# Kernel tuning notes

Hardware: AMD Instinct MI355X
Metric: run time of the kernel (lower is better)

Reference implementation:

```python
import jax, jax.numpy as jnp
from jax import lax
import numpy as np

WINDOW = 51
HALF = WINDOW // 2  # 25
K_SAUVOLA = 0.2     # skimage threshold_sauvola default k
RGB_W = np.array([0.2989, 0.5870, 0.1140], dtype=np.float32)  # tf.image.rgb_to_grayscale weights


def _window_sum(x, axis):
    """Sliding-window sum of length WINDOW along `axis`, 'same' size, reflect padding.
    O(1) per pixel via cumulative sums (integral-image style), matching the
    uniform_filter-based local statistics in skimage's Sauvola."""
    pad = [(0, 0)] * x.ndim
    pad[axis] = (HALF, HALF)
    xp = jnp.pad(x, pad, mode='reflect')
    cs = jnp.cumsum(xp, axis=axis)
    zshape = list(cs.shape)
    zshape[axis] = 1
    cs = jnp.concatenate([jnp.zeros(zshape, cs.dtype), cs], axis=axis)
    n = cs.shape[axis]
    hi = lax.slice_in_dim(cs, WINDOW, n, axis=axis)
    lo = lax.slice_in_dim(cs, 0, n - WINDOW, axis=axis)
    return hi - lo


def _box_mean(x):
    # separable 51x51 box filter over H (axis 1) and W (axis 2)
    s = _window_sum(_window_sum(x, axis=1), axis=2)
    return s / jnp.asarray(WINDOW * WINDOW, x.dtype)


def setup_inputs() -> dict:
    key = jax.random.key(0)
    inputs = jax.random.uniform(key, (8, 1024, 1024, 3), dtype=jnp.float32)
    return {"inputs": inputs}


def reference(inputs) -> jnp.ndarray:
    # RGB -> grayscale (channels == 3 branch), keep channel dim [B,H,W,1]
    gray = jnp.einsum('bhwc,c->bhw', inputs, jnp.asarray(RGB_W))[..., None]
    # local mean / std over 51x51 window
    m = _box_mean(gray)
    m2 = _box_mean(gray * gray)
    var = jnp.maximum(m2 - m * m, 0.0)
    s = jnp.sqrt(var)
    # skimage default dynamic range: r = 0.5 * (max - min) over the whole array
    r = 0.5 * (jnp.max(gray) - jnp.min(gray))
    thresh = m * (1.0 + K_SAUVOLA * (s / r - 1.0))
    # (gray > thresh) * 1
    return (gray > thresh).astype(jnp.float32)
```

## Files before the change

### kernel.cpp

```cpp
#include <hip/hip_runtime.h>

#define IMW 1024
#define IMH 1024
#define NB  8
#define HALF 25
#define STRIP 16
#define NCELL 64

#define W_R ((double)0.2989f)
#define W_G ((double)0.5870f)
#define W_B ((double)0.1140f)
#define INV_AREA (1.0 / 2601.0)

__device__ __forceinline__ int refl(int i, int n) {
    if (i < 0) i = -i;
    if (i >= n) i = 2 * n - 2 - i;
    return i;
}

__device__ __forceinline__ double wsum(const double* __restrict__ C, int p) {
    int a = p + HALF; if (a > IMW - 1) a = IMW - 1;
    int b = p - HALF - 1;
    double s = C[a] - (b >= 0 ? C[b] : 0.0);
    if (p <= HALF - 1)      s += C[HALF - p] - C[0];
    if (p >= IMW - HALF)    s += C[IMW - 2] - C[2*IMW - 2 - HALF - 1 - p];
    return s;
}

__global__ void k0_init(unsigned* cells) {
    cells[threadIdx.x] = (threadIdx.x < NCELL) ? 0xFFFFFFFFu : 0u;
}

__global__ __launch_bounds__(256) void k1_rowpass(const float* __restrict__ in,
                                                  float2* __restrict__ hp,
                                                  float* __restrict__ gray,
                                                  unsigned* __restrict__ cells) {
    __shared__ double cs1[IMW];
    __shared__ double cs2[IMW];
    __shared__ double wt1[4], wt2[4];
    __shared__ float bmin[4], bmax[4];
    const int row = blockIdx.x;
    const long long base = (long long)row * IMW;
    const int t = threadIdx.x;
    const int lane = t & 63, w = t >> 6;

    const float4* p4 = (const float4*)(in + base * 3);
    float4 f0 = p4[3*t], f1 = p4[3*t+1], f2 = p4[3*t+2];
    double g0 = (double)f0.x*W_R + (double)f0.y*W_G + (double)f0.z*W_B;
    double g1 = (double)f0.w*W_R + (double)f1.x*W_G + (double)f1.y*W_B;
    double g2 = (double)f1.z*W_R + (double)f1.w*W_G + (double)f2.x*W_B;
    double g3 = (double)f2.y*W_R + (double)f2.z*W_G + (double)f2.w*W_B;
    float gf0 = (float)g0, gf1 = (float)g1, gf2 = (float)g2, gf3 = (float)g3;

    ((float4*)(gray + base))[t] = make_float4(gf0, gf1, gf2, gf3);

    double l1_0 = g0, l1_1 = l1_0 + g1, l1_2 = l1_1 + g2, l1_3 = l1_2 + g3;
    double l2_0 = g0*g0, l2_1 = l2_0 + g1*g1, l2_2 = l2_1 + g2*g2, l2_3 = l2_2 + g3*g3;

    float lmin = fminf(fminf(gf0, gf1), fminf(gf2, gf3));
    float lmax = fmaxf(fmaxf(gf0, gf1), fmaxf(gf2, gf3));
    for (int off = 32; off; off >>= 1) {
        lmin = fminf(lmin, __shfl_down(lmin, off));
        lmax = fmaxf(lmax, __shfl_down(lmax, off));
    }
    if (lane == 0) { bmin[w] = lmin; bmax[w] = lmax; }

    double v1 = l1_3, v2 = l2_3;
    for (int off = 1; off < 64; off <<= 1) {
        double u1 = __shfl_up(v1, off);
        double u2 = __shfl_up(v2, off);
        if (lane >= off) { v1 += u1; v2 += u2; }
    }
    if (lane == 63) { wt1[w] = v1; wt2[w] = v2; }
    __syncthreads();
    double e1 = v1 - l1_3, e2 = v2 - l2_3;
    for (int j = 0; j < w; j++) { e1 += wt1[j]; e2 += wt2[j]; }

    double2* c1 = (double2*)&cs1[4*t];
    double2* c2 = (double2*)&cs2[4*t];
    c1[0] = make_double2(e1 + l1_0, e1 + l1_1);
    c1[1] = make_double2(e1 + l1_2, e1 + l1_3);
    c2[0] = make_double2(e2 + l2_0, e2 + l2_1);
    c2[1] = make_double2(e2 + l2_2, e2 + l2_3);

    if (t == 0) {
        float m0 = fminf(fminf(bmin[0], bmin[1]), fminf(bmin[2], bmin[3]));
        float m1 = fmaxf(fmaxf(bmax[0], bmax[1]), fmaxf(bmax[2], bmax[3]));
        int cell = row & (NCELL - 1);
        atomicMin(&cells[cell], __float_as_uint(m0));
        atomicMax(&cells[NCELL + cell], __float_as_uint(m1));
    }
    __syncthreads();

    for (int k = 0; k < 2; k++) {
        int p = 2*t + 512*k;
        float4 h = make_float4((float)wsum(cs1, p),   (float)wsum(cs2, p),
                               (float)wsum(cs1, p+1), (float)wsum(cs2, p+1));
        ((float4*)hp)[(base + p) >> 1] = h;
    }
}

__global__ __launch_bounds__(256) void k2_colpass(const float* __restrict__ gray,
                                                  const float2* __restrict__ hp,
                                                  const unsigned* __restrict__ cells,
                                                  float* __restrict__ out) {
    __shared__ double sr[2];
    const int t = threadIdx.x;
    if (t < 64) {
        unsigned mn = cells[t];
        unsigned mx = cells[NCELL + t];
        for (int off = 32; off; off >>= 1) {
            unsigned a = __shfl_down(mn, off);
            unsigned b = __shfl_down(mx, off);
            mn = (a < mn) ? a : mn;
            mx = (b > mx) ? b : mx;
        }
        if (t == 0) {
            sr[0] = (double)__uint_as_float(mn);
            sr[1] = (double)__uint_as_float(mx);
        }
    }
    __syncthreads();
    const double r  = 0.5 * (sr[1] - sr[0]);
    const double r2 = r * r;

    const int id   = blockIdx.x;
    const int b    = id & 7;
    const int rest = id >> 3;
    const int ys   = rest & 63;
    const int xc   = rest >> 6;
    const int x  = xc * 256 + t;
    const int y0 = ys * STRIP;
    const long long ib = (long long)b * IMH * IMW;

    double vx = 0.0, vy = 0.0;
    #pragma unroll 8
    for (int j = -HALF; j <= HALF; j++) {
        int ry = refl(y0 + j, IMH);
        float2 h = hp[ib + (long long)ry * IMW + x];
        vx += (double)h.x; vy += (double)h.y;
    }

    #pragma unroll 8
    for (int y = y0; y < y0 + STRIP; y++) {
        long long pix = ib + (long long)y * IMW + x;
        double g = (double)gray[pix];

        double m  = vx * INV_AREA;
        double va = fmax(vy * INV_AREA - m * m, 0.0);
        double A  = g - 0.8 * m;
        int o = (A > 0.0) && (A * A * r2 > 0.04 * m * m * va);
        out[pix] = o ? 1.0f : 0.0f;

        int ra = refl(y + HALF + 1, IMH);
        int rs = refl(y - HALF, IMH);
        float2 ha = hp[ib + (long long)ra * IMW + x];
        float2 hs = hp[ib + (long long)rs * IMW + x];
        vx += (double)ha.x - (double)hs.x;
        vy += (double)ha.y - (double)hs.y;
    }
}

extern "C" void kernel_launch(void* const* d_in, const int* in_sizes, int n_in,
                              void* d_out, int out_size, void* d_ws, size_t ws_size,
                              hipStream_t stream) {
    const float* in = (const float*)d_in[0];
    float* out = (float*)d_out;

    unsigned* cells = (unsigned*)d_ws;
    float2* hp = (float2*)((char*)d_ws + 4096);
    float* gray = (float*)((char*)d_ws + 4096
                           + (size_t)NB * IMH * IMW * sizeof(float2));

    hipLaunchKernelGGL(k0_init, dim3(1), dim3(2 * NCELL), 0, stream, cells);
    hipLaunchKernelGGL(k1_rowpass, dim3(NB * IMH), dim3(256), 0, stream,
                       in, hp, gray, cells);
    hipLaunchKernelGGL(k2_colpass, dim3((IMW / 256) * (IMH / STRIP) * NB), dim3(256), 0, stream,
                       gray, hp, cells, out);
}
```

Before: 221.1 us.

## Replace row prefix-scan with per-wave sliding window sums, four rows per block

The row pass now gives each wavefront its own image row and four rows to each block. The row is staged in swizzled shared memory as float, and each lane computes a running 51-wide window sum over its 16 pixels by direct summation plus incremental add/subtract. This replaces the block-wide double-precision prefix scan, its shuffles, and the two __syncthreads. The column pass strip height doubles to 32 rows, halving the redundant 51-row warmup per strip at the cost of fewer blocks. Each lane now does a 51-term warmup sum, which adds redundant arithmetic and some bank pressure.

```diff
diff --git a/kernel.cpp b/kernel.cpp
--- a/kernel.cpp
+++ b/kernel.cpp
@@ -4,8 +4,9 @@
 #define IMH 1024
 #define NB  8
 #define HALF 25
-#define STRIP 16
+#define STRIP 32
 #define NCELL 64
+#define RPB 4
 
 #define W_R ((double)0.2989f)
 #define W_G ((double)0.5870f)
@@ -18,14 +19,7 @@
     return i;
 }
 
-__device__ __forceinline__ double wsum(const double* __restrict__ C, int p) {
-    int a = p + HALF; if (a > IMW - 1) a = IMW - 1;
-    int b = p - HALF - 1;
-    double s = C[a] - (b >= 0 ? C[b] : 0.0);
-    if (p <= HALF - 1)      s += C[HALF - p] - C[0];
-    if (p >= IMW - HALF)    s += C[IMW - 2] - C[2*IMW - 2 - HALF - 1 - p];
-    return s;
-}
+__device__ __forceinline__ int swz(int p) { return p + (p >> 5); }
 
 __global__ void k0_init(unsigned* cells) {
     cells[threadIdx.x] = (threadIdx.x < NCELL) ? 0xFFFFFFFFu : 0u;
@@ -35,68 +29,72 @@
                                                   float2* __restrict__ hp,
                                                   float* __restrict__ gray,
                                                   unsigned* __restrict__ cells) {
-    __shared__ double cs1[IMW];
-    __shared__ double cs2[IMW];
-    __shared__ double wt1[4], wt2[4];
-    __shared__ float bmin[4], bmax[4];
-    const int row = blockIdx.x;
-    const long long base = (long long)row * IMW;
+    __shared__ float gb[RPB][1056];
     const int t = threadIdx.x;
     const int lane = t & 63, w = t >> 6;
+    const int row = blockIdx.x * RPB + w;
+    const long long base = (long long)row * IMW;
+    const int p0 = lane * 16;
 
     const float4* p4 = (const float4*)(in + base * 3);
-    float4 f0 = p4[3*t], f1 = p4[3*t+1], f2 = p4[3*t+2];
-    double g0 = (double)f0.x*W_R + (double)f0.y*W_G + (double)f0.z*W_B;
-    double g1 = (double)f0.w*W_R + (double)f1.x*W_G + (double)f1.y*W_B;
-    double g2 = (double)f1.z*W_R + (double)f1.w*W_G + (double)f2.x*W_B;
-    double g3 = (double)f2.y*W_R + (double)f2.z*W_G + (double)f2.w*W_B;
-    float gf0 = (float)g0, gf1 = (float)g1, gf2 = (float)g2, gf3 = (float)g3;
+    float lmin = 1e30f, lmax = -1e30f;
+    #pragma unroll
+    for (int q = 0; q < 4; q++) {
+        float4 f0 = p4[12*lane + 3*q + 0];
+        float4 f1 = p4[12*lane + 3*q + 1];
+        float4 f2 = p4[12*lane + 3*q + 2];
+        float g0 = (float)((double)f0.x*W_R + (double)f0.y*W_G + (double)f0.z*W_B);
+        float g1 = (float)((double)f0.w*W_R + (double)f1.x*W_G + (double)f1.y*W_B);
+        float g2 = (float)((double)f1.z*W_R + (double)f1.w*W_G + (double)f2.x*W_B);
+        float g3 = (float)((double)f2.y*W_R + (double)f2.z*W_G + (double)f2.w*W_B);
+        int p = p0 + 4*q;
+        gb[w][swz(p+0)] = g0; gb[w][swz(p+1)] = g1;
+        gb[w][swz(p+2)] = g2; gb[w][swz(p+3)] = g3;
+        ((float4*)(gray + base + p0))[q] = make_float4(g0, g1, g2, g3);
+        lmin = fminf(lmin, fminf(fminf(g0, g1), fminf(g2, g3)));
+        lmax = fmaxf(lmax, fmaxf(fmaxf(g0, g1), fmaxf(g2, g3)));
+    }
 
-    ((float4*)(gray + base))[t] = make_float4(gf0, gf1, gf2, gf3);
-
-    double l1_0 = g0, l1_1 = l1_0 + g1, l1_2 = l1_1 + g2, l1_3 = l1_2 + g3;
-    double l2_0 = g0*g0, l2_1 = l2_0 + g1*g1, l2_2 = l2_1 + g2*g2, l2_3 = l2_2 + g3*g3;
-
-    float lmin = fminf(fminf(gf0, gf1), fminf(gf2, gf3));
-    float lmax = fmaxf(fmaxf(gf0, gf1), fmaxf(gf2, gf3));
     for (int off = 32; off; off >>= 1) {
         lmin = fminf(lmin, __shfl_down(lmin, off));
         lmax = fmaxf(lmax, __shfl_down(lmax, off));
     }
-    if (lane == 0) { bmin[w] = lmin; bmax[w] = lmax; }
+    if (lane == 0) {
+        int cell = row & (NCELL - 1);
+        atomicMin(&cells[cell], __float_as_uint(lmin));
+        atomicMax(&cells[NCELL + cell], __float_as_uint(lmax));
+    }
 
-    double v1 = l1_3, v2 = l2_3;
-    for (int off = 1; off < 64; off <<= 1) {
-        double u1 = __shfl_up(v1, off);
-        double u2 = __shfl_up(v2, off);
-        if (lane >= off) { v1 += u1; v2 += u2; }
-    }
-    if (lane == 63) { wt1[w] = v1; wt2[w] = v2; }
-    __syncthreads();
-    double e1 = v1 - l1_3, e2 = v2 - l2_3;
-    for (int j = 0; j < w; j++) { e1 += wt1[j]; e2 += wt2[j]; }
-
-    double2* c1 = (double2*)&cs1[4*t];
-    double2* c2 = (double2*)&cs2[4*t];
-    c1[0] = make_double2(e1 + l1_0, e1 + l1_1);
-    c1[1] = make_double2(e1 + l1_2, e1 + l1_3);
-    c2[0] = make_double2(e2 + l2_0, e2 + l2_1);
-    c2[1] = make_double2(e2 + l2_2, e2 + l2_3);
-
-    if (t == 0) {
-        float m0 = fminf(fminf(bmin[0], bmin[1]), fminf(bmin[2], bmin[3]));
-        float m1 = fmaxf(fmaxf(bmax[0], bmax[1]), fmaxf(bmax[2], bmax[3]));
-        int cell = row & (NCELL - 1);
-        atomicMin(&cells[cell], __float_as_uint(m0));
-        atomicMax(&cells[NCELL + cell], __float_as_uint(m1));
-    }
     __syncthreads();
 
-    for (int k = 0; k < 2; k++) {
-        int p = 2*t + 512*k;
-        float4 h = make_float4((float)wsum(cs1, p),   (float)wsum(cs2, p),
-                               (float)wsum(cs1, p+1), (float)wsum(cs2, p+1));
-        ((float4*)hp)[(base + p) >> 1] = h;
+    double s1a = 0.0, s1b = 0.0, s1c = 0.0;
+    double s2a = 0.0, s2b = 0.0, s2c = 0.0;
+    #pragma unroll
+    for (int i = 0; i < 51; i += 3) {
+        double d0 = (double)gb[w][swz(refl(p0 - HALF + i + 0, IMW))];
+        double d1 = (double)gb[w][swz(refl(p0 - HALF + i + 1, IMW))];
+        double d2 = (double)gb[w][swz(refl(p0 - HALF + i + 2, IMW))];
+        s1a += d0; s2a = fma(d0, d0, s2a);
+        s1b += d1; s2b = fma(d1, d1, s2b);
+        s1c += d2; s2c = fma(d2, d2, s2c);
+    }
+    double v1 = (s1a + s1b) + s1c;
+    double v2 = (s2a + s2b) + s2c;
+
+    float4* hp4 = (float4*)(hp + base + p0);
+    float hx0 = 0.f, hy0 = 0.f;
+    #pragma unroll
+    for (int j = 0; j < 16; j++) {
+        float hx = (float)v1, hy = (float)v2;
+        if (j & 1) hp4[j >> 1] = make_float4(hx0, hy0, hx, hy);
+        else { hx0 = hx; hy0 = hy; }
+        if (j != 15) {
+            int p = p0 + j;
+            double ga = (double)gb[w][swz(refl(p + HALF + 1, IMW))];
+            double gs = (double)gb[w][swz(refl(p - HALF,     IMW))];
+            v1 += ga - gs;
+            v2 += ga * ga - gs * gs;
+        }
     }
 }
 
@@ -127,8 +125,8 @@
     const int id   = blockIdx.x;
     const int b    = id & 7;
     const int rest = id >> 3;
-    const int ys   = rest & 63;
-    const int xc   = rest >> 6;
+    const int ys   = rest & 31;
+    const int xc   = rest >> 5;
     const int x  = xc * 256 + t;
     const int y0 = ys * STRIP;
     const long long ib = (long long)b * IMH * IMW;
@@ -173,7 +171,7 @@
                            + (size_t)NB * IMH * IMW * sizeof(float2));
 
     hipLaunchKernelGGL(k0_init, dim3(1), dim3(2 * NCELL), 0, stream, cells);
-    hipLaunchKernelGGL(k1_rowpass, dim3(NB * IMH), dim3(256), 0, stream,
+    hipLaunchKernelGGL(k1_rowpass, dim3(NB * IMH / RPB), dim3(256), 0, stream,
                        in, hp, gray, cells);
     hipLaunchKernelGGL(k2_colpass, dim3((IMW / 256) * (IMH / STRIP) * NB), dim3(256), 0, stream,
                        gray, hp, cells, out);
```

After: 228.0 us. 1.03x slower.

## Pad shared cumsum arrays, double column strip height, fast-path interior strips

Applied to the files above, without the earlier changes.

The row pass pads the shared double cumulative-sum arrays (two doubles every eight) to cut LDS bank conflicts, and writes one float2 per thread per step instead of float4 pairs. The column pass doubles the strip height, which halves the 51-row warm-up reads per output row. Interior strips now use pointer-stepped loads with no reflect index math, while edge strips keep the reflect path. Taller strips halve the number of column-pass blocks, which lowers parallelism.

```diff
diff --git a/kernel.cpp b/kernel.cpp
--- a/kernel.cpp
+++ b/kernel.cpp
@@ -4,7 +4,7 @@
 #define IMH 1024
 #define NB  8
 #define HALF 25
-#define STRIP 16
+#define STRIP 32
 #define NCELL 64
 
 #define W_R ((double)0.2989f)
@@ -18,12 +18,14 @@
     return i;
 }
 
+__device__ __forceinline__ int pidx(int i) { return i + 2 * (i >> 3); }
+
 __device__ __forceinline__ double wsum(const double* __restrict__ C, int p) {
     int a = p + HALF; if (a > IMW - 1) a = IMW - 1;
     int b = p - HALF - 1;
-    double s = C[a] - (b >= 0 ? C[b] : 0.0);
-    if (p <= HALF - 1)      s += C[HALF - p] - C[0];
-    if (p >= IMW - HALF)    s += C[IMW - 2] - C[2*IMW - 2 - HALF - 1 - p];
+    double s = C[pidx(a)] - (b >= 0 ? C[pidx(b)] : 0.0);
+    if (p <= HALF - 1)      s += C[pidx(HALF - p)] - C[pidx(0)];
+    if (p >= IMW - HALF)    s += C[pidx(IMW - 2)] - C[pidx(2*IMW - 2 - HALF - 1 - p)];
     return s;
 }
 
@@ -35,8 +37,8 @@
                                                   float2* __restrict__ hp,
                                                   float* __restrict__ gray,
                                                   unsigned* __restrict__ cells) {
-    __shared__ double cs1[IMW];
-    __shared__ double cs2[IMW];
+    __shared__ double cs1[1280];
+    __shared__ double cs2[1280];
     __shared__ double wt1[4], wt2[4];
     __shared__ float bmin[4], bmax[4];
     const int row = blockIdx.x;
@@ -76,8 +78,9 @@
     double e1 = v1 - l1_3, e2 = v2 - l2_3;
     for (int j = 0; j < w; j++) { e1 += wt1[j]; e2 += wt2[j]; }
 
-    double2* c1 = (double2*)&cs1[4*t];
-    double2* c2 = (double2*)&cs2[4*t];
+    const int ci = 4 * t + 2 * (t >> 1);
+    double2* c1 = (double2*)&cs1[ci];
+    double2* c2 = (double2*)&cs2[ci];
     c1[0] = make_double2(e1 + l1_0, e1 + l1_1);
     c1[1] = make_double2(e1 + l1_2, e1 + l1_3);
     c2[0] = make_double2(e2 + l2_0, e2 + l2_1);
@@ -92,11 +95,9 @@
     }
     __syncthreads();
 
-    for (int k = 0; k < 2; k++) {
-        int p = 2*t + 512*k;
-        float4 h = make_float4((float)wsum(cs1, p),   (float)wsum(cs2, p),
-                               (float)wsum(cs1, p+1), (float)wsum(cs2, p+1));
-        ((float4*)hp)[(base + p) >> 1] = h;
+    for (int k = 0; k < 4; k++) {
+        int p = t + 256 * k;
+        hp[base + p] = make_float2((float)wsum(cs1, p), (float)wsum(cs2, p));
     }
 }
 
@@ -127,37 +128,67 @@
     const int id   = blockIdx.x;
     const int b    = id & 7;
     const int rest = id >> 3;
-    const int ys   = rest & 63;
-    const int xc   = rest >> 6;
+    const int ys   = rest & 31;
+    const int xc   = rest >> 5;
     const int x  = xc * 256 + t;
     const int y0 = ys * STRIP;
     const long long ib = (long long)b * IMH * IMW;
 
     double vx = 0.0, vy = 0.0;
-    #pragma unroll 8
-    for (int j = -HALF; j <= HALF; j++) {
-        int ry = refl(y0 + j, IMH);
-        float2 h = hp[ib + (long long)ry * IMW + x];
-        vx += (double)h.x; vy += (double)h.y;
-    }
-
-    #pragma unroll 8
-    for (int y = y0; y < y0 + STRIP; y++) {
-        long long pix = ib + (long long)y * IMW + x;
-        double g = (double)gray[pix];
-
-        double m  = vx * INV_AREA;
-        double va = fmax(vy * INV_AREA - m * m, 0.0);
-        double A  = g - 0.8 * m;
-        int o = (A > 0.0) && (A * A * r2 > 0.04 * m * m * va);
-        out[pix] = o ? 1.0f : 0.0f;
-
-        int ra = refl(y + HALF + 1, IMH);
-        int rs = refl(y - HALF, IMH);
-        float2 ha = hp[ib + (long long)ra * IMW + x];
-        float2 hs = hp[ib + (long long)rs * IMW + x];
-        vx += (double)ha.x - (double)hs.x;
-        vy += (double)ha.y - (double)hs.y;
+
+    if (ys >= 1 && ys <= 30) {
+        const float2* ph = hp + ib + (long long)(y0 - HALF) * IMW + x;
+        #pragma unroll 17
+        for (int j = 0; j < 51; j++) {
+            float2 h = ph[0];
+            vx += (double)h.x; vy += (double)h.y;
+            ph += IMW;
+        }
+        const float2* pa = hp + ib + (long long)(y0 + HALF + 1) * IMW + x;
+        const float2* ps = hp + ib + (long long)(y0 - HALF) * IMW + x;
+        const float*  pg = gray + ib + (long long)y0 * IMW + x;
+        float*        po = out  + ib + (long long)y0 * IMW + x;
+        #pragma unroll 8
+        for (int i = 0; i < STRIP; i++) {
+            float2 ha = pa[0];
+            float2 hs = ps[0];
+            double g = (double)pg[0];
+
+            double m  = vx * INV_AREA;
+            double va = fmax(vy * INV_AREA - m * m, 0.0);
+            double A  = g - 0.8 * m;
+            int o = (A > 0.0) && (A * A * r2 > 0.04 * m * m * va);
+            po[0] = o ? 1.0f : 0.0f;
+
+            vx += (double)ha.x - (double)hs.x;
+            vy += (double)ha.y - (double)hs.y;
+            pa += IMW; ps += IMW; pg += IMW; po += IMW;
+        }
+    } else {
+        #pragma unroll 8
+        for (int j = -HALF; j <= HALF; j++) {
+            int ry = refl(y0 + j, IMH);
+            float2 h = hp[ib + (long long)ry * IMW + x];
+            vx += (double)h.x; vy += (double)h.y;
+        }
+        #pragma unroll 8
+        for (int y = y0; y < y0 + STRIP; y++) {
+            long long pix = ib + (long long)y * IMW + x;
+            double g = (double)gray[pix];
+
+            double m  = vx * INV_AREA;
+            double va = fmax(vy * INV_AREA - m * m, 0.0);
+            double A  = g - 0.8 * m;
+            int o = (A > 0.0) && (A * A * r2 > 0.04 * m * m * va);
+            out[pix] = o ? 1.0f : 0.0f;
+
+            int ra = refl(y + HALF + 1, IMH);
+            int rs = refl(y - HALF, IMH);
+            float2 ha = hp[ib + (long long)ra * IMW + x];
+            float2 hs = hp[ib + (long long)rs * IMW + x];
+            vx += (double)ha.x - (double)hs.x;
+            vy += (double)ha.y - (double)hs.y;
+        }
     }
 }
 
```

Result: faster. 208.7 us (-5.6%).
